# Performance work log

Hardware: AMD Instinct MI355X
Metric: run time of the kernel (lower is better)

Reference implementation:

```python
import jax, jax.numpy as jnp
import numpy as np

B, S, Q, C = 1, 128, 256, 256
H, DH = 8, 32
TOT = H * DH  # 256


def setup_inputs() -> dict:
    key = jax.random.key(0)
    ks = jax.random.split(key, 12)
    inp = {
        'q_x': jax.random.normal(ks[0], (B, S, Q, C), jnp.float32),
        'kv_x': jax.random.normal(ks[1], (B, S, Q, C), jnp.float32),
        'bias_mask': jax.random.normal(ks[2], (B, S, 1, 1, Q), jnp.float32),
        'bias_pair': jax.random.normal(ks[3], (B, 1, H, Q, Q), jnp.float32),
        # torch nn.Linear weights are (out_features, in_features)
        'Wq': jax.random.normal(ks[4], (TOT, C), jnp.float32) * (C ** -0.5),
        'Wk': jax.random.normal(ks[5], (TOT, C), jnp.float32) * (C ** -0.5),
        'Wv': jax.random.normal(ks[6], (TOT, C), jnp.float32) * (C ** -0.5),
        'Wg': jax.random.normal(ks[7], (TOT, C), jnp.float32) * 0.02,
        'bg': jnp.ones((TOT,), jnp.float32),   # 'gating' init: zero W, bias=1
        'Wo': jax.random.normal(ks[8], (C, TOT), jnp.float32) * 0.02,
        'bo': jnp.zeros((C,), jnp.float32),
    }
    return inp


def reference(q_x, kv_x, bias_mask, bias_pair, Wq, Wk, Wv, Wg, bg, Wo, bo):
    # QKV projections (no bias), split heads, move head dim before Q: [B,S,H,Q,DH]
    def proj(x, W):
        y = jnp.einsum('bsqc,dc->bsqd', x, W)
        return y.reshape(*y.shape[:-1], H, DH).transpose(0, 1, 3, 2, 4)

    q = proj(q_x, Wq)   # NOTE: literal source applies NO 1/sqrt(dh) scaling in naive mode
    k = proj(kv_x, Wk)
    v = proj(kv_x, Wv)

    # scores [B,S,H,Q,K] with additive biases, manual softmax
    scores = jnp.einsum('bshqd,bshkd->bshqk', q, k) + bias_mask + bias_pair
    a = jax.nn.softmax(scores, axis=-1)
    o = jnp.einsum('bshqk,bshkd->bshqd', a, v)
    o = o.transpose(0, 1, 3, 2, 4)  # [B,S,Q,H,DH]

    # gating
    g = jax.nn.sigmoid(jnp.einsum('bsqc,dc->bsqd', q_x, Wg) + bg)
    o = o * g.reshape(*g.shape[:-1], H, DH)

    # output projection
    o = o.reshape(*o.shape[:-2], TOT)
    return jnp.einsum('bsqd,cd->bsqc', o, Wo) + bo
```

## Files before the change

### kernel.cpp

```cpp
#include <hip/hip_runtime.h>


typedef unsigned short u16;
typedef unsigned int   u32;
typedef float  f32x4  __attribute__((ext_vector_type(4)));
typedef __bf16 bf16x8 __attribute__((ext_vector_type(8)));

__device__ __forceinline__ float bf2f(u16 u) {
    union { u32 i; float f; } v; v.i = ((u32)u) << 16; return v.f;
}
__device__ __forceinline__ u16 f2bf(float f) {
    __bf16 h = (__bf16)f; return __builtin_bit_cast(u16, h);
}

__device__ __forceinline__ void gld16(const u16* g, u16* l) {
    __builtin_amdgcn_global_load_lds(
        (const __attribute__((address_space(1))) u32*)g,
        (__attribute__((address_space(3))) u32*)l, 16, 0, 0);
}

__device__ __forceinline__ size_t hm(int row, int col) {
    const int s = row >> 8, q = row & 255, h = col >> 5, dh = col & 31;
    return ((size_t)((h * 128 + s) * 256 + q) << 5) + dh;
}

__device__ __forceinline__ void cvt8(const float4* src, u16* dst) {
    float4 a = src[0], b = src[1];
    u16 r[8];
    r[0] = f2bf(a.x); r[1] = f2bf(a.y); r[2] = f2bf(a.z); r[3] = f2bf(a.w);
    r[4] = f2bf(b.x); r[5] = f2bf(b.y); r[6] = f2bf(b.z); r[7] = f2bf(b.w);
    *(uint4*)dst = *(uint4*)r;
}

__global__ __launch_bounds__(256) void prep(
    const float* __restrict__ Wq, const float* __restrict__ Wk,
    const float* __restrict__ Wv, const float* __restrict__ Wg,
    const float* __restrict__ Wo, const float* __restrict__ bp,
    u16* __restrict__ Wball, float* __restrict__ bppf)
{
    const int b = blockIdx.x, t = threadIdx.x;
    if (b < 160) {
        const int mat = b >> 5;
        const float* W = (mat == 0) ? Wq : (mat == 1) ? Wk : (mat == 2) ? Wv
                       : (mat == 3) ? Wg : Wo;
        const int off = (b & 31) * 2048 + t * 8;
        cvt8((const float4*)(W + off), Wball + mat * 65536 + off);
    } else {
        const int b3 = b - 160;
        const int u0 = (b3 * 256 + t) * 2;
        #pragma unroll
        for (int k2 = 0; k2 < 2; ++k2) {
            const int u  = u0 + k2;
            const int l  = u & 63;
            const int nt = (u >> 6) & 15;
            const int tt = u >> 10;
            const int ww = tt & 3, qqt = (tt >> 2) & 3, hh = tt >> 4;
            const int q  = qqt * 64 + ww * 16 + (l & 15);
            const int kp = nt * 16 + (l >> 4) * 4;
            const float4 v = *(const float4*)(bp + (size_t)(hh * 256 + q) * 256 + kp);
            *(float4*)(bppf + (size_t)u * 4) = v;
        }
    }
}

__global__ __launch_bounds__(256) void proj_all(
    const float* __restrict__ Xqf, const float* __restrict__ Xkvf,
    const u16* __restrict__ Wball, const float* __restrict__ bg,
    u16* __restrict__ Qh, u16* __restrict__ Kh, u16* __restrict__ Vh, u16* __restrict__ Gh)
{
    __shared__ u16 At[128 * 256];
    __shared__ u16 Wt[128 * 256];

    const int bid = blockIdx.x;
    const int mb  = bid & 255;
    const int nb  = bid >> 8;
    const int t   = nb >> 1;
    const int n0  = (nb & 1) * 128;
    const int m0  = mb * 128;
    const float* Af = (t == 0 || t == 3) ? Xqf : Xkvf;
    const u16* W = Wball + t * 65536;
    u16*       O = (t == 0) ? Qh : (t == 1) ? Kh : (t == 2) ? Vh : Gh;

    const int tid  = threadIdx.x;
    const int lane = tid & 63;
    const int w    = tid >> 6;
    const int quad = lane >> 4;
    const int ln   = lane & 15;
    const int wm   = (w >> 1) * 64;
    const int wn   = (w & 1) * 64;
    const int lrow  = lane >> 3;
    const int lcol  = (lane & 7) * 8;
    const int lrow2 = lane >> 5;
    const int lcol2 = (lane & 31) * 8;

    #pragma unroll
    for (int qq = 0; qq < 16; ++qq) {
        const int r = w * 32 + qq * 2;
        gld16(W + (size_t)(n0 + r + lrow2) * 256 + lcol2, &Wt[r * 256]);
    }
    #pragma unroll
    for (int it = 0; it < 16; ++it) {
        const int row = w * 32 + (it & 3) * 8 + lrow;
        const int col = (it >> 2) * 64 + lcol;
        cvt8((const float4*)(Af + (size_t)(m0 + row) * 256 + col),
             &At[row * 256 + col]);
    }
    __syncthreads();

    f32x4 acc[4][4] = {};
    #pragma unroll
    for (int kk = 0; kk < 8; ++kk) {
        const int kc = kk * 32 + quad * 8;
        bf16x8 af[4], bfr[4];
        #pragma unroll
        for (int i = 0; i < 4; ++i)
            af[i] = __builtin_bit_cast(bf16x8, *(const uint4*)&At[(wm + i * 16 + ln) * 256 + kc]);
        #pragma unroll
        for (int j = 0; j < 4; ++j)
            bfr[j] = __builtin_bit_cast(bf16x8, *(const uint4*)&Wt[(wn + j * 16 + ln) * 256 + kc]);
        #pragma unroll
        for (int i = 0; i < 4; ++i)
            #pragma unroll
            for (int j = 0; j < 4; ++j)
                acc[i][j] = __builtin_amdgcn_mfma_f32_16x16x32_bf16(bfr[j], af[i], acc[i][j], 0, 0, 0);
    }

    const int act = (t == 3);
    #pragma unroll
    for (int i = 0; i < 4; ++i) {
        const int row = m0 + wm + i * 16 + ln;
        #pragma unroll
        for (int j = 0; j < 4; ++j) {
            const int colb = n0 + wn + j * 16 + quad * 4;
            u16 r4[4];
            if (act) {
                const float4 bgv = *(const float4*)&bg[colb];
                float v0 = acc[i][j][0] + bgv.x;
                float v1 = acc[i][j][1] + bgv.y;
                float v2 = acc[i][j][2] + bgv.z;
                float v3 = acc[i][j][3] + bgv.w;
                r4[0] = f2bf(1.0f / (1.0f + __expf(-v0)));
                r4[1] = f2bf(1.0f / (1.0f + __expf(-v1)));
                r4[2] = f2bf(1.0f / (1.0f + __expf(-v2)));
                r4[3] = f2bf(1.0f / (1.0f + __expf(-v3)));
            } else {
                r4[0] = f2bf(acc[i][j][0]);
                r4[1] = f2bf(acc[i][j][1]);
                r4[2] = f2bf(acc[i][j][2]);
                r4[3] = f2bf(acc[i][j][3]);
            }
            *(uint2*)(O + hm(row, colb)) = *(const uint2*)r4;
        }
    }
}

__global__ __launch_bounds__(256) void gemm_out(
    const u16* __restrict__ Oh, const u16* __restrict__ Wob,
    const float* __restrict__ bo, float* __restrict__ out)
{
    __shared__ u16 At[64 * 64];
    __shared__ u16 Wt[128 * 64];

    const int bid = blockIdx.x;
    const int m0  = (bid & 511) * 64;
    const int n0  = (bid >> 9) * 128;

    const int tid  = threadIdx.x;
    const int lane = tid & 63;
    const int w    = tid >> 6;
    const int quad = lane >> 4;
    const int ln   = lane & 15;
    const int wm   = (w >> 1) * 32;
    const int wn   = (w & 1) * 64;
    const int lrow = lane >> 3;
    const int lcol = (lane & 7) * 8;

    f32x4 acc[2][4] = {};

    for (int k0 = 0; k0 < 256; k0 += 64) {
        __syncthreads();
        #pragma unroll
        for (int qq = 0; qq < 2; ++qq) {
            const int r = w * 16 + qq * 8;
            gld16(Oh + hm(m0 + r + lrow, k0 + lcol), &At[r * 64]);
        }
        #pragma unroll
        for (int qq = 0; qq < 4; ++qq) {
            const int r = w * 32 + qq * 8;
            gld16(Wob + (size_t)(n0 + r + lrow) * 256 + k0 + lcol, &Wt[r * 64]);
        }
        __syncthreads();

        #pragma unroll
        for (int kk = 0; kk < 2; ++kk) {
            const int kc = kk * 32 + quad * 8;
            bf16x8 af[2], bfr[4];
            #pragma unroll
            for (int i = 0; i < 2; ++i)
                af[i] = __builtin_bit_cast(bf16x8, *(const uint4*)&At[(wm + i * 16 + ln) * 64 + kc]);
            #pragma unroll
            for (int j = 0; j < 4; ++j)
                bfr[j] = __builtin_bit_cast(bf16x8, *(const uint4*)&Wt[(wn + j * 16 + ln) * 64 + kc]);
            #pragma unroll
            for (int i = 0; i < 2; ++i)
                #pragma unroll
                for (int j = 0; j < 4; ++j)
                    acc[i][j] = __builtin_amdgcn_mfma_f32_16x16x32_bf16(bfr[j], af[i], acc[i][j], 0, 0, 0);
        }
    }

    #pragma unroll
    for (int i = 0; i < 2; ++i) {
        const int row = m0 + wm + i * 16 + ln;
        #pragma unroll
        for (int j = 0; j < 4; ++j) {
            const int colb = n0 + wn + j * 16 + quad * 4;
            const float4 bov = *(const float4*)&bo[colb];
            float4 o;
            o.x = acc[i][j][0] + bov.x;
            o.y = acc[i][j][1] + bov.y;
            o.z = acc[i][j][2] + bov.z;
            o.w = acc[i][j][3] + bov.w;
            *(float4*)&out[(size_t)row * 256 + colb] = o;
        }
    }
}

__global__ __launch_bounds__(256, 2) void attn_kernel(
    const u16* __restrict__ Qh, const u16* __restrict__ Kh, const u16* __restrict__ Vh,
    const u16* __restrict__ Gh, const float* __restrict__ bm, const float* __restrict__ bppf,
    u16* __restrict__ Oh)
{
    __shared__ u16   Vt[32][264];
    __shared__ u16   Pl[4][16][76];
    __shared__ float bmf[256];

    const int hs   = blockIdx.x;
    const int h    = hs & 7;
    const int s    = hs >> 3;
    const int tid  = threadIdx.x;
    const int lane = tid & 63;
    const int w    = tid >> 6;
    const int quad = lane >> 4;
    const int ln   = lane & 15;

    const size_t hsBase = ((size_t)(h * 128 + s) * 256) << 5;

    {
        const uint4* vp = (const uint4*)(Vh + hsBase + (size_t)tid * 32);
        uint4 vv0 = vp[0], vv1 = vp[1], vv2 = vp[2], vv3 = vp[3];
        u16 tmp[32];
        *(uint4*)&tmp[0]  = vv0; *(uint4*)&tmp[8]  = vv1;
        *(uint4*)&tmp[16] = vv2; *(uint4*)&tmp[24] = vv3;
        #pragma unroll
        for (int dh = 0; dh < 32; ++dh) Vt[dh][tid] = tmp[dh];
        bmf[tid] = bm[s * 256 + tid];
    }
    __syncthreads();

    for (int iq = 0; iq < 4; ++iq) {
        const int qt = iq;
        const int q0 = qt * 64 + w * 16;

        bf16x8 aq = __builtin_bit_cast(bf16x8,
            *(const uint4*)(Qh + hsBase + (size_t)(q0 + ln) * 32 + quad * 8));

        const size_t obase = hsBase + (size_t)(q0 + ln) * 32;
        const uint2 ga = *(const uint2*)(Gh + obase + quad * 4);
        const uint2 gb = *(const uint2*)(Gh + obase + 16 + quad * 4);

        const float* bpt = bppf + ((size_t)(((h * 4 + qt) * 4 + w) * 16) * 64 + lane) * 4;

        f32x4 sc[16];
        float rmax[4] = {-1e30f, -1e30f, -1e30f, -1e30f};
        #pragma unroll
        for (int c = 0; c < 4; ++c) {
            bf16x8 bk[4];
            f32x4  bv[4];
            #pragma unroll
            for (int j = 0; j < 4; ++j) {
                const int nt = c * 4 + j;
                bk[j] = __builtin_bit_cast(bf16x8,
                    *(const uint4*)(Kh + hsBase + (size_t)(nt * 16 + ln) * 32 + quad * 8));
                bv[j] = *(const f32x4*)(bpt + (size_t)nt * 256);
            }
            #pragma unroll
            for (int j = 0; j < 4; ++j) {
                const int nt = c * 4 + j;
                f32x4 z = {0.f, 0.f, 0.f, 0.f};
                f32x4 r = __builtin_amdgcn_mfma_f32_16x16x32_bf16(bk[j], aq, z, 0, 0, 0);
                const f32x4 bm4 = *(const f32x4*)&bmf[nt * 16 + quad * 4];
                #pragma unroll
                for (int rr = 0; rr < 4; ++rr) {
                    float v = r[rr] + bm4[rr] + bv[j][rr];
                    sc[nt][rr] = v;
                    rmax[rr] = fmaxf(rmax[rr], v);
                }
            }
            __builtin_amdgcn_sched_barrier(0);
        }

        float m = fmaxf(fmaxf(rmax[0], rmax[1]), fmaxf(rmax[2], rmax[3]));
        m = fmaxf(m, __shfl_xor(m, 16));
        m = fmaxf(m, __shfl_xor(m, 32));

        float s4[4] = {0.f, 0.f, 0.f, 0.f};
        #pragma unroll
        for (int nt = 0; nt < 16; ++nt)
            #pragma unroll
            for (int rr = 0; rr < 4; ++rr) {
                float p = __expf(sc[nt][rr] - m);
                sc[nt][rr] = p;
                s4[rr] += p;
            }
        float tsum = (s4[0] + s4[1]) + (s4[2] + s4[3]);
        tsum += __shfl_xor(tsum, 16);
        tsum += __shfl_xor(tsum, 32);
        const float rinv = 1.0f / tsum;

        f32x4 o0 = {0.f, 0.f, 0.f, 0.f}, o1 = {0.f, 0.f, 0.f, 0.f};
        #pragma unroll
        for (int c = 0; c < 4; ++c) {
            #pragma unroll
            for (int ntl = 0; ntl < 4; ++ntl) {
                const int nt = c * 4 + ntl;
                u16 r4[4];
                #pragma unroll
                for (int rr = 0; rr < 4; ++rr)
                    r4[rr] = f2bf(sc[nt][rr] * rinv);
                *(uint2*)&Pl[w][ln][ntl * 16 + quad * 4] = *(const uint2*)r4;
            }
            #pragma unroll
            for (int kcl = 0; kcl < 2; ++kcl) {
                bf16x8 pa = __builtin_bit_cast(bf16x8, *(const uint4*)&Pl[w][ln][kcl * 32 + quad * 8]);
                bf16x8 v0 = __builtin_bit_cast(bf16x8, *(const uint4*)&Vt[ln][c * 64 + kcl * 32 + quad * 8]);
                bf16x8 v1 = __builtin_bit_cast(bf16x8, *(const uint4*)&Vt[16 + ln][c * 64 + kcl * 32 + quad * 8]);
                o0 = __builtin_amdgcn_mfma_f32_16x16x32_bf16(v0, pa, o0, 0, 0, 0);
                o1 = __builtin_amdgcn_mfma_f32_16x16x32_bf16(v1, pa, o1, 0, 0, 0);
            }
        }

        const u16* gau = (const u16*)&ga;
        const u16* gbu = (const u16*)&gb;
        u16 ra[4], rb[4];
        #pragma unroll
        for (int rr = 0; rr < 4; ++rr) {
            ra[rr] = f2bf(o0[rr] * bf2f(gau[rr]));
            rb[rr] = f2bf(o1[rr] * bf2f(gbu[rr]));
        }
        *(uint2*)(Oh + obase + quad * 4)      = *(const uint2*)ra;
        *(uint2*)(Oh + obase + 16 + quad * 4) = *(const uint2*)rb;
    }
}

extern "C" void kernel_launch(void* const* d_in, const int* in_sizes, int n_in,
                              void* d_out, int out_size, void* d_ws, size_t ws_size,
                              hipStream_t stream)
{
    const float* qx  = (const float*)d_in[0];
    const float* kvx = (const float*)d_in[1];
    const float* bm  = (const float*)d_in[2];
    const float* bp  = (const float*)d_in[3];
    const float* Wq  = (const float*)d_in[4];
    const float* Wk  = (const float*)d_in[5];
    const float* Wv  = (const float*)d_in[6];
    const float* Wg  = (const float*)d_in[7];
    const float* bg  = (const float*)d_in[8];
    const float* Wo  = (const float*)d_in[9];
    const float* bo  = (const float*)d_in[10];
    float* out = (float*)d_out;

    const size_t NEL = (size_t)32768 * 256;
    u16* Qh = (u16*)d_ws;
    u16* Kh = Qh + NEL;
    u16* Vh = Kh + NEL;
    u16* Gh = Vh + NEL;
    u16* Wball = Gh + NEL;
    float* bppf = (float*)(Wball + 5 * 65536);

    prep<<<dim3(416), dim3(256), 0, stream>>>(Wq, Wk, Wv, Wg, Wo, bp, Wball, bppf);

    proj_all<<<dim3(2048), dim3(256), 0, stream>>>(qx, kvx, Wball, bg, Qh, Kh, Vh, Gh);

    attn_kernel<<<dim3(1024), dim3(256), 0, stream>>>(Qh, Kh, Vh, Gh, bm, bppf, Qh );

    gemm_out<<<dim3(1024), dim3(256), 0, stream>>>(Qh , Wball + 4 * 65536, bo, out);
}
```

Before: 242.4 us.

## Load GEMM operands directly from global memory into registers, dropping LDS staging

The projection and output GEMM kernels no longer stage A and W tiles in shared memory. Each lane now loads its MFMA fragments straight from global memory, converting fp32 inputs to bf16 in registers, and sched_barriers keep the per-k-step loads grouped. The block order in proj_all is also permuted so the tiles that read q_x (Q and G) and those that read kv_x (K and V) run next to each other, which should improve L2 reuse. This removes the LDS footprint and the block barriers, which may raise occupancy. The cost is redundant global and L2 traffic, since each operand row is now loaded by several waves, and partial-row access that coalesces less well.

Result: slower. 270.5 us (+11.6%).

```diff
diff --git a/kernel.cpp b/kernel.cpp
--- a/kernel.cpp
+++ b/kernel.cpp
@@ -11,12 +11,6 @@
 }
 __device__ __forceinline__ u16 f2bf(float f) {
     __bf16 h = (__bf16)f; return __builtin_bit_cast(u16, h);
-}
-
-__device__ __forceinline__ void gld16(const u16* g, u16* l) {
-    __builtin_amdgcn_global_load_lds(
-        (const __attribute__((address_space(1))) u32*)g,
-        (__attribute__((address_space(3))) u32*)l, 16, 0, 0);
 }
 
 __device__ __forceinline__ size_t hm(int row, int col) {
@@ -30,6 +24,14 @@
     r[0] = f2bf(a.x); r[1] = f2bf(a.y); r[2] = f2bf(a.z); r[3] = f2bf(a.w);
     r[4] = f2bf(b.x); r[5] = f2bf(b.y); r[6] = f2bf(b.z); r[7] = f2bf(b.w);
     *(uint4*)dst = *(uint4*)r;
+}
+
+__device__ __forceinline__ bf16x8 ldcvt8(const float* ap) {
+    float4 a = *(const float4*)ap, b = *(const float4*)(ap + 4);
+    u16 r[8];
+    r[0] = f2bf(a.x); r[1] = f2bf(a.y); r[2] = f2bf(a.z); r[3] = f2bf(a.w);
+    r[4] = f2bf(b.x); r[5] = f2bf(b.y); r[6] = f2bf(b.z); r[7] = f2bf(b.w);
+    return __builtin_bit_cast(bf16x8, *(uint4*)r);
 }
 
 __global__ __launch_bounds__(256) void prep(
@@ -68,18 +70,17 @@
     const u16* __restrict__ Wball, const float* __restrict__ bg,
     u16* __restrict__ Qh, u16* __restrict__ Kh, u16* __restrict__ Vh, u16* __restrict__ Gh)
 {
-    __shared__ u16 At[128 * 256];
-    __shared__ u16 Wt[128 * 256];
-
     const int bid = blockIdx.x;
     const int mb  = bid & 255;
     const int nb  = bid >> 8;
     const int t   = nb >> 1;
     const int n0  = (nb & 1) * 128;
     const int m0  = mb * 128;
-    const float* Af = (t == 0 || t == 3) ? Xqf : Xkvf;
-    const u16* W = Wball + t * 65536;
-    u16*       O = (t == 0) ? Qh : (t == 1) ? Kh : (t == 2) ? Vh : Gh;
+    const float* Af = (t <= 1) ? Xqf : Xkvf;
+    const int mat = (t == 0) ? 0 : (t == 1) ? 3 : (t == 2) ? 1 : 2;
+    const u16* W = Wball + mat * 65536;
+    u16*       O = (t == 0) ? Qh : (t == 1) ? Gh : (t == 2) ? Kh : Vh;
+    const int act = (t == 1);
 
     const int tid  = threadIdx.x;
     const int lane = tid & 63;
@@ -88,44 +89,28 @@
     const int ln   = lane & 15;
     const int wm   = (w >> 1) * 64;
     const int wn   = (w & 1) * 64;
-    const int lrow  = lane >> 3;
-    const int lcol  = (lane & 7) * 8;
-    const int lrow2 = lane >> 5;
-    const int lcol2 = (lane & 31) * 8;
-
-    #pragma unroll
-    for (int qq = 0; qq < 16; ++qq) {
-        const int r = w * 32 + qq * 2;
-        gld16(W + (size_t)(n0 + r + lrow2) * 256 + lcol2, &Wt[r * 256]);
-    }
-    #pragma unroll
-    for (int it = 0; it < 16; ++it) {
-        const int row = w * 32 + (it & 3) * 8 + lrow;
-        const int col = (it >> 2) * 64 + lcol;
-        cvt8((const float4*)(Af + (size_t)(m0 + row) * 256 + col),
-             &At[row * 256 + col]);
-    }
-    __syncthreads();
 
     f32x4 acc[4][4] = {};
+
     #pragma unroll
     for (int kk = 0; kk < 8; ++kk) {
         const int kc = kk * 32 + quad * 8;
         bf16x8 af[4], bfr[4];
         #pragma unroll
         for (int i = 0; i < 4; ++i)
-            af[i] = __builtin_bit_cast(bf16x8, *(const uint4*)&At[(wm + i * 16 + ln) * 256 + kc]);
+            af[i] = ldcvt8(Af + (size_t)(m0 + wm + i * 16 + ln) * 256 + kc);
         #pragma unroll
         for (int j = 0; j < 4; ++j)
-            bfr[j] = __builtin_bit_cast(bf16x8, *(const uint4*)&Wt[(wn + j * 16 + ln) * 256 + kc]);
+            bfr[j] = __builtin_bit_cast(bf16x8,
+                *(const uint4*)(W + (size_t)(n0 + wn + j * 16 + ln) * 256 + kc));
         #pragma unroll
         for (int i = 0; i < 4; ++i)
             #pragma unroll
             for (int j = 0; j < 4; ++j)
                 acc[i][j] = __builtin_amdgcn_mfma_f32_16x16x32_bf16(bfr[j], af[i], acc[i][j], 0, 0, 0);
-    }
-
-    const int act = (t == 3);
+        __builtin_amdgcn_sched_barrier(0);
+    }
+
     #pragma unroll
     for (int i = 0; i < 4; ++i) {
         const int row = m0 + wm + i * 16 + ln;
@@ -158,9 +143,6 @@
     const u16* __restrict__ Oh, const u16* __restrict__ Wob,
     const float* __restrict__ bo, float* __restrict__ out)
 {
-    __shared__ u16 At[64 * 64];
-    __shared__ u16 Wt[128 * 64];
-
     const int bid = blockIdx.x;
     const int m0  = (bid & 511) * 64;
     const int n0  = (bid >> 9) * 128;
@@ -172,41 +154,27 @@
     const int ln   = lane & 15;
     const int wm   = (w >> 1) * 32;
     const int wn   = (w & 1) * 64;
-    const int lrow = lane >> 3;
-    const int lcol = (lane & 7) * 8;
 
     f32x4 acc[2][4] = {};
 
-    for (int k0 = 0; k0 < 256; k0 += 64) {
-        __syncthreads();
-        #pragma unroll
-        for (int qq = 0; qq < 2; ++qq) {
-            const int r = w * 16 + qq * 8;
-            gld16(Oh + hm(m0 + r + lrow, k0 + lcol), &At[r * 64]);
-        }
-        #pragma unroll
-        for (int qq = 0; qq < 4; ++qq) {
-            const int r = w * 32 + qq * 8;
-            gld16(Wob + (size_t)(n0 + r + lrow) * 256 + k0 + lcol, &Wt[r * 64]);
-        }
-        __syncthreads();
-
-        #pragma unroll
-        for (int kk = 0; kk < 2; ++kk) {
-            const int kc = kk * 32 + quad * 8;
-            bf16x8 af[2], bfr[4];
-            #pragma unroll
-            for (int i = 0; i < 2; ++i)
-                af[i] = __builtin_bit_cast(bf16x8, *(const uint4*)&At[(wm + i * 16 + ln) * 64 + kc]);
+    #pragma unroll
+    for (int kk = 0; kk < 8; ++kk) {
+        const int kc = kk * 32 + quad * 8;
+        bf16x8 af[2], bfr[4];
+        #pragma unroll
+        for (int i = 0; i < 2; ++i)
+            af[i] = __builtin_bit_cast(bf16x8,
+                *(const uint4*)(Oh + hm(m0 + wm + i * 16 + ln, kc)));
+        #pragma unroll
+        for (int j = 0; j < 4; ++j)
+            bfr[j] = __builtin_bit_cast(bf16x8,
+                *(const uint4*)(Wob + (size_t)(n0 + wn + j * 16 + ln) * 256 + kc));
+        #pragma unroll
+        for (int i = 0; i < 2; ++i)
             #pragma unroll
             for (int j = 0; j < 4; ++j)
-                bfr[j] = __builtin_bit_cast(bf16x8, *(const uint4*)&Wt[(wn + j * 16 + ln) * 64 + kc]);
-            #pragma unroll
-            for (int i = 0; i < 2; ++i)
-                #pragma unroll
-                for (int j = 0; j < 4; ++j)
-                    acc[i][j] = __builtin_amdgcn_mfma_f32_16x16x32_bf16(bfr[j], af[i], acc[i][j], 0, 0, 0);
-        }
+                acc[i][j] = __builtin_amdgcn_mfma_f32_16x16x32_bf16(bfr[j], af[i], acc[i][j], 0, 0, 0);
+        __builtin_amdgcn_sched_barrier(0);
     }
 
     #pragma unroll
```
